# Kernel tuning notes

Measured on AMD Instinct MI355X. Metric: run time of the kernel, lower is better.

The kernel has to match this reference:

```python
import jax, jax.numpy as jnp
import numpy as np

EPS = 1.1920929e-07  # torch fp32 finfo eps (F.rms_norm default)

def apply_rotary_emb(x, cos, sin):
    # x: [..., L, hd]; cos/sin: [L, hd/2] broadcast over leading dims
    x1, x2 = jnp.split(x, 2, axis=-1)
    y1 = x1 * cos + x2 * sin
    y2 = -x1 * sin + x2 * cos
    return jnp.concatenate([y1, y2], axis=-1)

def rms_norm(x):
    ms = jnp.mean(x * x, axis=-1, keepdims=True)
    return x * jax.lax.rsqrt(ms + EPS)

def setup_inputs() -> dict:
    key = jax.random.key(0)
    ks = jax.random.split(key, 7)
    B, L, D, H = 4, 2048, 2048, 16
    hd = D // H
    x = jax.random.normal(ks[0], (B, L, D), dtype=jnp.float32)
    cos = jax.random.uniform(ks[1], (L, hd // 2), dtype=jnp.float32)
    sin = jax.random.uniform(ks[2], (L, hd // 2), dtype=jnp.float32)
    s = 1.0 / np.sqrt(D)
    Wq = jax.random.normal(ks[3], (D, D), dtype=jnp.float32) * s
    Wk = jax.random.normal(ks[4], (hd, D), dtype=jnp.float32) * s
    Wv = jax.random.normal(ks[5], (hd, D), dtype=jnp.float32) * s
    Wo = jax.random.normal(ks[6], (D, D), dtype=jnp.float32) * s
    return {"x": x, "cos": cos, "sin": sin, "Wq": Wq, "Wk": Wk, "Wv": Wv, "Wo": Wo}

def reference(x, cos, sin, Wq, Wk, Wv, Wo):
    B, L, D = x.shape
    hd = Wk.shape[0]
    H = D // hd
    q = (x @ Wq.T).reshape(B, L, H, hd).transpose(0, 2, 1, 3)   # [B,H,L,hd]
    k = x @ Wk.T                                                 # [B,L,hd] single KV head
    v = x @ Wv.T                                                 # [B,L,hd]
    q = rms_norm(apply_rotary_emb(q, cos, sin))
    k = rms_norm(apply_rotary_emb(k, cos, sin))
    new_k = k[:, None]  # [B,1,L,hd] cache layout
    new_v = v[:, None]
    scale = 1.0 / np.sqrt(hd).astype(np.float32)
    scores = jnp.einsum('bhqd,bkd->bhqk', q, k) * scale          # [B,H,L,L]
    causal = jnp.tril(jnp.ones((L, L), dtype=bool))
    scores = jnp.where(causal, scores, -jnp.inf)
    attn = jax.nn.softmax(scores, axis=-1)
    out = jnp.einsum('bhqk,bkd->bhqd', attn, v)                  # [B,H,L,hd]
    out = out.transpose(0, 2, 1, 3).reshape(B, L, D) @ Wo.T
    return (out, (new_k, new_v))
```

## Files before the change

kernel.cpp:

```cpp
#include <hip/hip_runtime.h>
#include <hip/hip_bf16.h>

typedef __hip_bfloat16 bf16;
typedef __attribute__((ext_vector_type(8))) short s8v;
typedef __attribute__((ext_vector_type(4))) short s4v;
typedef __attribute__((ext_vector_type(4))) float f4v;

#define B_  4
#define L_  2048
#define D_  2048
#define H_  16
#define HD_ 128

#define QSCALE 0.12751745f

__device__ __forceinline__ float ldm(const void* p, size_t i, int m) {
    return m ? ((const float*)p)[i]
             : __bfloat162float(((const bf16*)p)[i]);
}
__device__ __forceinline__ void stm(void* p, size_t i, int m, float v) {
    if (m) ((float*)p)[i] = v;
    else   ((bf16*)p)[i] = __float2bfloat16(v);
}

__device__ __forceinline__ void glds16(const bf16* g, bf16* l) {
    __builtin_amdgcn_global_load_lds(
        (const __attribute__((address_space(1))) void*)g,
        (__attribute__((address_space(3))) void*)l, 16, 0, 0);
}

__global__ __launch_bounds__(256) void cvt_kernel(
    const void* __restrict__ src, bf16* __restrict__ dst, int n8, int m)
{
    int i = blockIdx.x * 256 + threadIdx.x;
    if (i >= n8) return;
    if (m) {
        const f4v* p = (const f4v*)src + (size_t)i * 2;
        f4v a = p[0], b = p[1];
        bf16 t[8];
        #pragma unroll
        for (int e = 0; e < 4; e++) {
            t[e]     = __float2bfloat16(a[e]);
            t[4 + e] = __float2bfloat16(b[e]);
        }
        ((s8v*)dst)[i] = *(s8v*)&t[0];
    } else {
        ((s8v*)dst)[i] = ((const s8v*)src)[i];
    }
}

__global__ __launch_bounds__(256) void gemm_glds_kernel(
    const bf16* __restrict__ A, const bf16* __restrict__ Bw,
    void* __restrict__ C, size_t cOff, int cm, int N, int K)
{
    __shared__ bf16 a_lds[128 * 32];
    __shared__ bf16 b_lds[128 * 32];
    const int t = threadIdx.x;

    const int nbx = gridDim.x;
    const int id  = blockIdx.y * nbx + blockIdx.x;
    const int cpx = (nbx * (int)gridDim.y) >> 3;
    const int swz = (id & 7) * cpx + (id >> 3);
    const int n0  = (swz % nbx) * 128;
    const int m0  = (swz / nbx) * 128;

    const int w  = t >> 6, ln = t & 63;
    const int wr = w >> 1, wc = w & 1;
    const int fr = ln & 15, kg = ln >> 4;

    const int srow = w * 32 + (ln >> 2);
    const int scol = (ln & 3) * 8;
    const bf16* ga = A  + (size_t)(m0 + srow) * K + scol;
    const bf16* gb = Bw + (size_t)(n0 + srow) * K + scol;
    bf16* la = &a_lds[w * 1024];
    bf16* lb = &b_lds[w * 1024];

    f4v acc[4][4];
    #pragma unroll
    for (int i = 0; i < 4; i++)
        #pragma unroll
        for (int j = 0; j < 4; j++)
            #pragma unroll
            for (int r = 0; r < 4; r++) acc[i][j][r] = 0.f;

    for (int k0 = 0; k0 < K; k0 += 32) {
        __syncthreads();
        glds16(ga + k0,          la);
        glds16(ga + k0 + 16 * K, la + 512);
        glds16(gb + k0,          lb);
        glds16(gb + k0 + 16 * K, lb + 512);
        __syncthreads();

        s8v af[4], bfv[4];
        #pragma unroll
        for (int i = 0; i < 4; i++)
            af[i] = *(const s8v*)&a_lds[(wr * 64 + i * 16 + fr) * 32 + kg * 8];
        #pragma unroll
        for (int j = 0; j < 4; j++)
            bfv[j] = *(const s8v*)&b_lds[(wc * 64 + j * 16 + fr) * 32 + kg * 8];
        #pragma unroll
        for (int i = 0; i < 4; i++)
            #pragma unroll
            for (int j = 0; j < 4; j++)
                acc[i][j] = __builtin_amdgcn_mfma_f32_16x16x32_bf16(
                    af[i], bfv[j], acc[i][j], 0, 0, 0);
    }

    #pragma unroll
    for (int i = 0; i < 4; i++)
        #pragma unroll
        for (int j = 0; j < 4; j++)
            #pragma unroll
            for (int r = 0; r < 4; r++) {
                int row = m0 + wr * 64 + i * 16 + kg * 4 + r;
                int col = n0 + wc * 64 + j * 16 + fr;
                stm(C, cOff + (size_t)row * N + col, cm, acc[i][j][r]);
            }
}

__global__ __launch_bounds__(512, 2) void gemm256_kernel(
    const bf16* __restrict__ A, const bf16* __restrict__ Bw,
    void* __restrict__ C, size_t cOff, int cm, int N, int K)
{
    __shared__ __align__(16) bf16 a_lds[2][256 * 64];
    __shared__ __align__(16) bf16 b_lds[2][256 * 64];
    const int t = threadIdx.x;

    const int nbx = gridDim.x;
    const int id  = blockIdx.y * nbx + blockIdx.x;
    const int cpx = (nbx * (int)gridDim.y) >> 3;
    const int swz = (id & 7) * cpx + (id >> 3);
    const int n0  = (swz % nbx) * 256;
    const int m0  = (swz / nbx) * 256;

    const int w  = t >> 6, ln = t & 63;
    const int wr = w >> 2, wc = w & 3;
    const int fr = ln & 15, kg = ln >> 4;

    const int sb   = w * 256 + ln;
    const int srow = sb >> 3;
    const int scol = (sb & 7) * 8;
    const bf16* gA = A  + (size_t)(m0 + srow) * K + scol;
    const bf16* gB = Bw + (size_t)(n0 + srow) * K + scol;
    const int lbase = w * 2048;

    f4v acc[8][4];
    #pragma unroll
    for (int i = 0; i < 8; i++)
        #pragma unroll
        for (int j = 0; j < 4; j++)
            #pragma unroll
            for (int r = 0; r < 4; r++) acc[i][j][r] = 0.f;

    const int NT = K >> 6;

    #pragma unroll
    for (int u = 0; u < 4; u++) {
        glds16(gA + (size_t)(u * 8) * K, &a_lds[0][lbase + u * 512]);
        glds16(gB + (size_t)(u * 8) * K, &b_lds[0][lbase + u * 512]);
    }

    for (int kt = 0; kt < NT; ++kt) {
        const int cur = kt & 1;
        if (kt + 1 < NT) {
            const int nk = (kt + 1) << 6;
            #pragma unroll
            for (int u = 0; u < 4; u++) {
                glds16(gA + (size_t)(u * 8) * K + nk, &a_lds[cur ^ 1][lbase + u * 512]);
                glds16(gB + (size_t)(u * 8) * K + nk, &b_lds[cur ^ 1][lbase + u * 512]);
            }
            asm volatile("s_waitcnt vmcnt(8)" ::: "memory");
        } else {
            asm volatile("s_waitcnt vmcnt(0)" ::: "memory");
        }
        __builtin_amdgcn_s_barrier();

        #pragma unroll
        for (int kst = 0; kst < 2; kst++) {
            s8v af[8], bf[4];
            #pragma unroll
            for (int i = 0; i < 8; i++)
                af[i] = *(const s8v*)&a_lds[cur][(wr * 128 + i * 16 + fr) * 64
                                                + kst * 32 + kg * 8];
            #pragma unroll
            for (int j = 0; j < 4; j++)
                bf[j] = *(const s8v*)&b_lds[cur][(wc * 64 + j * 16 + fr) * 64
                                                + kst * 32 + kg * 8];
            #pragma unroll
            for (int i = 0; i < 8; i++)
                #pragma unroll
                for (int j = 0; j < 4; j++)
                    acc[i][j] = __builtin_amdgcn_mfma_f32_16x16x32_bf16(
                        af[i], bf[j], acc[i][j], 0, 0, 0);
        }
        asm volatile("s_waitcnt lgkmcnt(0)" ::: "memory");
        __builtin_amdgcn_s_barrier();
    }

    #pragma unroll
    for (int i = 0; i < 8; i++)
        #pragma unroll
        for (int j = 0; j < 4; j++)
            #pragma unroll
            for (int r = 0; r < 4; r++) {
                int row = m0 + wr * 128 + i * 16 + kg * 4 + r;
                int col = n0 + wc * 64 + j * 16 + fr;
                stm(C, cOff + (size_t)row * N + col, cm, acc[i][j][r]);
            }
}

__global__ __launch_bounds__(256) void rot_rms_kernel(
    bf16* __restrict__ p, int stride, int ldiv, float oscale,
    const void* __restrict__ cosb, const void* __restrict__ sinb, int em,
    bf16* __restrict__ kout, void* __restrict__ out2, int om)
{
    const int row  = blockIdx.x * 4 + (threadIdx.x >> 6);
    const int lane = threadIdx.x & 63;
    const int l    = (row / ldiv) % L_;
    bf16* pr = p + (size_t)row * stride;

    float x1 = __bfloat162float(pr[lane]);
    float x2 = __bfloat162float(pr[lane + 64]);
    float c  = ldm(cosb, (size_t)l * 64 + lane, em);
    float s  = ldm(sinb, (size_t)l * 64 + lane, em);
    float y1 =  x1 * c + x2 * s;
    float y2 = -x1 * s + x2 * c;

    float sq = y1 * y1 + y2 * y2;
    #pragma unroll
    for (int off = 32; off > 0; off >>= 1) sq += __shfl_xor(sq, off);
    float rinv = rsqrtf(sq * (1.0f / 128.0f) + 1.1920929e-07f);
    y1 *= rinv; y2 *= rinv;

    pr[lane]      = __float2bfloat16(y1 * oscale);
    pr[lane + 64] = __float2bfloat16(y2 * oscale);
    if (kout) {
        kout[(size_t)row * HD_ + lane]      = __float2bfloat16(y1);
        kout[(size_t)row * HD_ + lane + 64] = __float2bfloat16(y2);
    }
    if (out2) {
        stm(out2, (size_t)row * HD_ + lane,      om, y1);
        stm(out2, (size_t)row * HD_ + lane + 64, om, y2);
    }
}

__global__ __launch_bounds__(256) void transpose_v_kernel(
    const bf16* __restrict__ v, int vstride, int vcol0,
    bf16* __restrict__ vt, void* __restrict__ vout, int om)
{
    const int l0 = blockIdx.x * 32, c0 = blockIdx.y * 32, b = blockIdx.z;
    __shared__ bf16 tile[32][36];
    const int t = threadIdx.x;
    {
        int r = t >> 3, c4 = (t & 7) * 4;
        const bf16* src = v + (size_t)(b * L_ + l0 + r) * vstride + vcol0 + c0 + c4;
        s4v sv = *(const s4v*)src;
        *(s4v*)&tile[r][c4] = sv;
        size_t oidx = (size_t)(b * L_ + l0 + r) * HD_ + c0 + c4;
        if (om) {
            f4v f;
            #pragma unroll
            for (int e = 0; e < 4; e++) f[e] = __bfloat162float(((bf16*)&sv)[e]);
            *(f4v*)((float*)vout + oidx) = f;
        } else {
            *(s4v*)((bf16*)vout + oidx) = sv;
        }
    }
    __syncthreads();
    {
        int c = t >> 3, r4 = (t & 7) * 4;
        bf16 tmp[4];
        #pragma unroll
        for (int e = 0; e < 4; e++) tmp[e] = tile[r4 + e][c];
        *(s4v*)&vt[(size_t)(b * HD_ + c0 + c) * L_ + l0 + r4] = *(s4v*)&tmp[0];
    }
}

__global__ __launch_bounds__(256, 2) void attn_kernel(
    const bf16* __restrict__ q,
    const bf16* __restrict__ kbuf,
    const bf16* __restrict__ vt,
    bf16* __restrict__ o)
{
    const int bx = blockIdx.x;
    const int h  = blockIdx.y, b = blockIdx.z;
    const int t  = threadIdx.x, w = t >> 6, ln = t & 63;
    const int fr = ln & 15, kg = ln >> 4;

    __shared__ bf16 k_lds[64][132];
    __shared__ bf16 vt_lds[128][68];
    __shared__ bf16 p_lds[128][68];

    const int rK = t >> 2, cK = (t & 3) * 32;
    const int rV = t >> 1, cV = (t & 1) * 32;

    #pragma unroll 1
    for (int half = 0; half < 2; half++) {
        const int l0 = half ? (L_ - 128 - bx * 128) : bx * 128;

        s8v qf[2][4];
        #pragma unroll
        for (int s = 0; s < 2; s++) {
            size_t base = (size_t)(b * L_ + l0 + w * 32 + s * 16 + fr) * D_
                          + h * HD_ + kg * 8;
            #pragma unroll
            for (int kst = 0; kst < 4; kst++)
                qf[s][kst] = *(const s8v*)(q + base + kst * 32);
        }

        float m_i[2] = {-3.0e38f, -3.0e38f};
        float l_i[2] = {0.f, 0.f};
        f4v o_acc[8][2];
        #pragma unroll
        for (int mt = 0; mt < 8; mt++)
            #pragma unroll
            for (int s = 0; s < 2; s++)
                #pragma unroll
                for (int r = 0; r < 4; r++) o_acc[mt][s][r] = 0.f;

        const int qmax_w = l0 + w * 32 + 31;
        const int kend   = l0 + 128;

        for (int kb = 0; kb < kend; kb += 64) {
            s8v kr[4], vr[4];
            {
                const s8v* ks = (const s8v*)(kbuf + (size_t)(b * L_ + kb + rK) * HD_ + cK);
                const s8v* vs = (const s8v*)(vt + (size_t)(b * HD_ + rV) * L_ + kb + cV);
                #pragma unroll
                for (int u = 0; u < 4; u++) { kr[u] = ks[u]; vr[u] = vs[u]; }
            }
            __syncthreads();
            #pragma unroll
            for (int u = 0; u < 4; u++) {
                *(s8v*)&k_lds[rK][cK + u * 8]  = kr[u];
                *(s8v*)&vt_lds[rV][cV + u * 8] = vr[u];
            }
            __syncthreads();

            if (kb <= qmax_w) {
                f4v sacc[4][2];
                #pragma unroll
                for (int jm = 0; jm < 4; jm++)
                    #pragma unroll
                    for (int s = 0; s < 2; s++)
                        #pragma unroll
                        for (int r = 0; r < 4; r++) sacc[jm][s][r] = 0.f;

                __builtin_amdgcn_s_setprio(1);
                #pragma unroll
                for (int kst = 0; kst < 4; kst++) {
                    #pragma unroll
                    for (int jm = 0; jm < 4; jm++) {
                        s8v af = *(const s8v*)&k_lds[jm * 16 + fr][kst * 32 + kg * 8];
                        #pragma unroll
                        for (int s = 0; s < 2; s++)
                            sacc[jm][s] = __builtin_amdgcn_mfma_f32_16x16x32_bf16(
                                af, qf[s][kst], sacc[jm][s], 0, 0, 0);
                    }
                }
                __builtin_amdgcn_s_setprio(0);

                #pragma unroll
                for (int s = 0; s < 2; s++) {
                    const int qrow = l0 + w * 32 + s * 16 + fr;
                    float sv[4][4];
                    if (kb + 63 > l0 + w * 32 + s * 16) {
                        #pragma unroll
                        for (int jm = 0; jm < 4; jm++)
                            #pragma unroll
                            for (int r = 0; r < 4; r++) {
                                int key = kb + jm * 16 + kg * 4 + r;
                                sv[jm][r] = (key <= qrow) ? sacc[jm][s][r] : -3.0e38f;
                            }
                    } else {
                        #pragma unroll
                        for (int jm = 0; jm < 4; jm++)
                            #pragma unroll
                            for (int r = 0; r < 4; r++) sv[jm][r] = sacc[jm][s][r];
                    }
                    float mj[4];
                    #pragma unroll
                    for (int jm = 0; jm < 4; jm++)
                        mj[jm] = fmaxf(fmaxf(sv[jm][0], sv[jm][1]),
                                       fmaxf(sv[jm][2], sv[jm][3]));
                    float mx = fmaxf(fmaxf(mj[0], mj[1]), fmaxf(mj[2], mj[3]));
                    mx = fmaxf(mx, __shfl_xor(mx, 16));
                    mx = fmaxf(mx, __shfl_xor(mx, 32));

                    float mn = m_i[s];
                    if (!__all(mx - mn <= 8.0f)) {
                        float mnew  = fmaxf(mn, mx);
                        float alpha = exp2f(mn - mnew);
                        m_i[s] = mnew;
                        l_i[s] *= alpha;
                        #pragma unroll
                        for (int mt = 0; mt < 8; mt++)
                            #pragma unroll
                            for (int r = 0; r < 4; r++) o_acc[mt][s][r] *= alpha;
                        mn = mnew;
                    }

                    float rs0 = 0.f, rs1 = 0.f;
                    #pragma unroll
                    for (int jm = 0; jm < 4; jm++) {
                        float p0 = exp2f(sv[jm][0] - mn);
                        float p1 = exp2f(sv[jm][1] - mn);
                        float p2 = exp2f(sv[jm][2] - mn);
                        float p3 = exp2f(sv[jm][3] - mn);
                        rs0 += p0 + p2;
                        rs1 += p1 + p3;
                        bf16 pb[4];
                        pb[0] = __float2bfloat16(p0);
                        pb[1] = __float2bfloat16(p1);
                        pb[2] = __float2bfloat16(p2);
                        pb[3] = __float2bfloat16(p3);
                        *(s4v*)&p_lds[w * 32 + s * 16 + fr][jm * 16 + kg * 4] =
                            *(s4v*)&pb[0];
                    }
                    float rsum = rs0 + rs1;
                    rsum += __shfl_xor(rsum, 16);
                    rsum += __shfl_xor(rsum, 32);
                    l_i[s] += rsum;
                }

                __builtin_amdgcn_s_setprio(1);
                #pragma unroll
                for (int ks2 = 0; ks2 < 2; ks2++) {
                    s8v pf[2];
                    #pragma unroll
                    for (int s = 0; s < 2; s++)
                        pf[s] = *(const s8v*)&p_lds[w * 32 + s * 16 + fr][ks2 * 32 + kg * 8];
                    #pragma unroll
                    for (int mt = 0; mt < 8; mt++) {
                        s8v vf = *(const s8v*)&vt_lds[mt * 16 + fr][ks2 * 32 + kg * 8];
                        #pragma unroll
                        for (int s = 0; s < 2; s++)
                            o_acc[mt][s] = __builtin_amdgcn_mfma_f32_16x16x32_bf16(
                                vf, pf[s], o_acc[mt][s], 0, 0, 0);
                    }
                }
                __builtin_amdgcn_s_setprio(0);
            }
        }

        #pragma unroll
        for (int s = 0; s < 2; s++) {
            float rl = 1.f / l_i[s];
            size_t base = (size_t)(b * L_ + l0 + w * 32 + s * 16 + fr) * D_
                          + h * HD_ + kg * 4;
            #pragma unroll
            for (int mt = 0; mt < 8; mt++) {
                bf16 ob[4];
                #pragma unroll
                for (int r = 0; r < 4; r++)
                    ob[r] = __float2bfloat16(o_acc[mt][s][r] * rl);
                *(s4v*)(o + base + mt * 16) = *(s4v*)&ob[0];
            }
        }
    }
}

extern "C" void kernel_launch(void* const* d_in, const int* in_sizes, int n_in,
                              void* d_out, int out_size, void* d_ws, size_t ws_size,
                              hipStream_t stream)
{
    const void* x    = d_in[0];
    const void* cosb = d_in[1];
    const void* sinb = d_in[2];
    const void* Wq   = d_in[3];
    const void* Wk   = d_in[4];
    const void* Wv   = d_in[5];
    const void* Wo   = d_in[6];

    const size_t NX   = (size_t)B_ * L_ * D_;
    const size_t NW   = (size_t)D_ * D_;
    const size_t NWK  = (size_t)HD_ * D_;
    const size_t NKV  = (size_t)B_ * L_ * HD_;
    const size_t NOUT = NX + 2 * NKV;

    const int xm  = (in_sizes[0] == (int)(NX * 2))  ? 0 : 1;
    const int em  = (in_sizes[1] == (int)((size_t)L_ * 64 * 2)) ? 0 : 1;
    const int wm  = (in_sizes[3] == (int)(NW * 2))  ? 0 : 1;
    const int wkm = (in_sizes[4] == (int)(NWK * 2)) ? 0 : 1;
    const int om  = (out_size    == (int)(NOUT * 2)) ? 0 : 1;

    bf16* qbuf  = (bf16*)d_ws;
    bf16* kvbuf = qbuf  + NX;
    bf16* kbuf  = kvbuf + (size_t)B_ * L_ * 256;
    bf16* vtbuf = kbuf  + NKV;
    bf16* wkvb  = vtbuf + NKV;
    bf16* wwb   = kvbuf;

    const bf16* xb;
    if (xm) {
        cvt_kernel<<<(int)(NX / 8 / 256), 256, 0, stream>>>(x, (bf16*)d_out, (int)(NX / 8), 1);
        xb = (const bf16*)d_out;
    } else {
        xb = (const bf16*)x;
    }

    const bf16* wq;
    if (wm) {
        cvt_kernel<<<(int)(NW / 8 / 256), 256, 0, stream>>>(Wq, wwb, (int)(NW / 8), 1);
        wq = wwb;
    } else {
        wq = (const bf16*)Wq;
    }
    cvt_kernel<<<(int)(NWK / 8 / 256), 256, 0, stream>>>(Wk, wkvb,       (int)(NWK / 8), wkm);
    cvt_kernel<<<(int)(NWK / 8 / 256), 256, 0, stream>>>(Wv, wkvb + NWK, (int)(NWK / 8), wkm);

    gemm256_kernel<<<dim3(D_ / 256, (B_ * L_) / 256), 512, 0, stream>>>(
        xb, wq, qbuf, 0, 0, D_, D_);
    gemm_glds_kernel<<<dim3(256 / 128, (B_ * L_) / 128), 256, 0, stream>>>(
        xb, wkvb, kvbuf, 0, 0, 256, D_);

    rot_rms_kernel<<<(B_ * L_ * H_) / 4, 256, 0, stream>>>(
        qbuf, HD_, H_, QSCALE, cosb, sinb, em, nullptr, nullptr, 0);
    char* d_out_b = (char*)d_out;
    void* kout2 = d_out_b + NX * (om ? 4 : 2);
    rot_rms_kernel<<<(B_ * L_) / 4, 256, 0, stream>>>(
        kvbuf, 256, 1, 1.0f, cosb, sinb, em, kbuf, kout2, om);

    void* vout2 = d_out_b + (NX + NKV) * (om ? 4 : 2);
    transpose_v_kernel<<<dim3(L_ / 32, HD_ / 32, B_), 256, 0, stream>>>(
        kvbuf, 256, 128, vtbuf, vout2, om);

    attn_kernel<<<dim3(L_ / 256, H_, B_), 256, 0, stream>>>(
        qbuf, kbuf, vtbuf, qbuf);

    const bf16* wo;
    if (wm) {
        cvt_kernel<<<(int)(NW / 8 / 256), 256, 0, stream>>>(Wo, wwb, (int)(NW / 8), 1);
        wo = wwb;
    } else {
        wo = (const bf16*)Wo;
    }
    gemm256_kernel<<<dim3(D_ / 256, (B_ * L_) / 256), 512, 0, stream>>>(
        qbuf, wo, d_out, 0, om, D_, D_);
}
```

Before: 521.4 us.

## Split GEMM K-tile into half-tiles with finer-grained staged prefetch

Restructures the 256x256 GEMM main loop so each 64-wide K tile is stored as two 32-wide halves, and global-to-LDS loads are issued per half-tile, interleaved between MFMA groups. Waits use vmcnt on outstanding half-tile units, and s_setprio brackets the MFMA bursts. The aim is to overlap memory loads with compute more evenly and reduce stalls at barriers. It adds more barriers and waitcnt bookkeeping, and the vmcnt counts must match the number of outstanding loads exactly or the loop will read stale data.

Measured after the change: 502.8 us. 1.04x faster.

```diff
diff --git a/kernel.cpp b/kernel.cpp
--- a/kernel.cpp
+++ b/kernel.cpp
@@ -118,12 +118,25 @@
             }
 }
 
+__device__ __forceinline__ void stage_unit(
+    const bf16* __restrict__ G, int row0, int k0, int K,
+    bf16* lds, int w, int ln)
+{
+    #pragma unroll
+    for (int u = 0; u < 2; u++) {
+        int blk = u * 8 + w;
+        int r   = blk * 16 + (ln >> 2);
+        int ck  = (ln & 3) * 8;
+        glds16(G + (size_t)(row0 + r) * K + k0 + ck, lds + blk * 512);
+    }
+}
+
 __global__ __launch_bounds__(512, 2) void gemm256_kernel(
     const bf16* __restrict__ A, const bf16* __restrict__ Bw,
     void* __restrict__ C, size_t cOff, int cm, int N, int K)
 {
-    __shared__ __align__(16) bf16 a_lds[2][256 * 64];
-    __shared__ __align__(16) bf16 b_lds[2][256 * 64];
+    __shared__ __align__(16) bf16 a_lds[2][2][256 * 32];
+    __shared__ __align__(16) bf16 b_lds[2][2][256 * 32];
     const int t = threadIdx.x;
 
     const int nbx = gridDim.x;
@@ -137,13 +150,6 @@
     const int wr = w >> 2, wc = w & 3;
     const int fr = ln & 15, kg = ln >> 4;
 
-    const int sb   = w * 256 + ln;
-    const int srow = sb >> 3;
-    const int scol = (sb & 7) * 8;
-    const bf16* gA = A  + (size_t)(m0 + srow) * K + scol;
-    const bf16* gB = Bw + (size_t)(n0 + srow) * K + scol;
-    const int lbase = w * 2048;
-
     f4v acc[8][4];
     #pragma unroll
     for (int i = 0; i < 8; i++)
@@ -154,47 +160,96 @@
 
     const int NT = K >> 6;
 
-    #pragma unroll
-    for (int u = 0; u < 4; u++) {
-        glds16(gA + (size_t)(u * 8) * K, &a_lds[0][lbase + u * 512]);
-        glds16(gB + (size_t)(u * 8) * K, &b_lds[0][lbase + u * 512]);
+    stage_unit(A,  m0, 0,  K, &a_lds[0][0][0], w, ln);
+    stage_unit(Bw, n0, 0,  K, &b_lds[0][0][0], w, ln);
+    stage_unit(A,  m0, 32, K, &a_lds[0][1][0], w, ln);
+    stage_unit(Bw, n0, 32, K, &b_lds[0][1][0], w, ln);
+    if (NT > 1) {
+        stage_unit(A,  m0, 64, K, &a_lds[1][0][0], w, ln);
+        stage_unit(Bw, n0, 64, K, &b_lds[1][0][0], w, ln);
     }
 
     for (int kt = 0; kt < NT; ++kt) {
-        const int cur = kt & 1;
-        if (kt + 1 < NT) {
-            const int nk = (kt + 1) << 6;
-            #pragma unroll
-            for (int u = 0; u < 4; u++) {
-                glds16(gA + (size_t)(u * 8) * K + nk, &a_lds[cur ^ 1][lbase + u * 512]);
-                glds16(gB + (size_t)(u * 8) * K + nk, &b_lds[cur ^ 1][lbase + u * 512]);
-            }
-            asm volatile("s_waitcnt vmcnt(8)" ::: "memory");
-        } else {
-            asm volatile("s_waitcnt vmcnt(0)" ::: "memory");
-        }
+        const int c = kt & 1, nb = c ^ 1;
+        if (kt + 1 < NT) asm volatile("s_waitcnt vmcnt(8)" ::: "memory");
+        else             asm volatile("s_waitcnt vmcnt(4)" ::: "memory");
         __builtin_amdgcn_s_barrier();
 
-        #pragma unroll
-        for (int kst = 0; kst < 2; kst++) {
-            s8v af[8], bf[4];
+        if (kt + 1 < NT)
+            stage_unit(A, m0, (kt + 1) * 64 + 32, K, &a_lds[nb][1][0], w, ln);
+        {
+            s8v af[8], bfv[4];
             #pragma unroll
             for (int i = 0; i < 8; i++)
-                af[i] = *(const s8v*)&a_lds[cur][(wr * 128 + i * 16 + fr) * 64
-                                                + kst * 32 + kg * 8];
-            #pragma unroll
-            for (int j = 0; j < 4; j++)
-                bf[j] = *(const s8v*)&b_lds[cur][(wc * 64 + j * 16 + fr) * 64
-                                                + kst * 32 + kg * 8];
+                af[i] = *(const s8v*)&a_lds[c][0][(wr * 128 + i * 16 + fr) * 32 + kg * 8];
+            #pragma unroll
+            for (int j = 0; j < 2; j++)
+                bfv[j] = *(const s8v*)&b_lds[c][0][(wc * 64 + j * 16 + fr) * 32 + kg * 8];
+            asm volatile("s_waitcnt lgkmcnt(0)" ::: "memory");
+            __builtin_amdgcn_s_setprio(1);
             #pragma unroll
             for (int i = 0; i < 8; i++)
                 #pragma unroll
-                for (int j = 0; j < 4; j++)
+                for (int j = 0; j < 2; j++)
                     acc[i][j] = __builtin_amdgcn_mfma_f32_16x16x32_bf16(
-                        af[i], bf[j], acc[i][j], 0, 0, 0);
-        }
-        asm volatile("s_waitcnt lgkmcnt(0)" ::: "memory");
+                        af[i], bfv[j], acc[i][j], 0, 0, 0);
+            __builtin_amdgcn_s_setprio(0);
+
+            if (kt + 1 < NT)
+                stage_unit(Bw, n0, (kt + 1) * 64 + 32, K, &b_lds[nb][1][0], w, ln);
+            #pragma unroll
+            for (int j = 2; j < 4; j++)
+                bfv[j] = *(const s8v*)&b_lds[c][0][(wc * 64 + j * 16 + fr) * 32 + kg * 8];
+            asm volatile("s_waitcnt lgkmcnt(0)" ::: "memory");
+            __builtin_amdgcn_s_setprio(1);
+            #pragma unroll
+            for (int i = 0; i < 8; i++)
+                #pragma unroll
+                for (int j = 2; j < 4; j++)
+                    acc[i][j] = __builtin_amdgcn_mfma_f32_16x16x32_bf16(
+                        af[i], bfv[j], acc[i][j], 0, 0, 0);
+            __builtin_amdgcn_s_setprio(0);
+        }
+
+        if (kt + 1 < NT) asm volatile("s_waitcnt vmcnt(8)" ::: "memory");
+        else             asm volatile("s_waitcnt vmcnt(0)" ::: "memory");
         __builtin_amdgcn_s_barrier();
+
+        if (kt + 2 < NT)
+            stage_unit(A, m0, (kt + 2) * 64, K, &a_lds[c][0][0], w, ln);
+        {
+            s8v af[8], bfv[4];
+            #pragma unroll
+            for (int i = 0; i < 8; i++)
+                af[i] = *(const s8v*)&a_lds[c][1][(wr * 128 + i * 16 + fr) * 32 + kg * 8];
+            #pragma unroll
+            for (int j = 0; j < 2; j++)
+                bfv[j] = *(const s8v*)&b_lds[c][1][(wc * 64 + j * 16 + fr) * 32 + kg * 8];
+            asm volatile("s_waitcnt lgkmcnt(0)" ::: "memory");
+            __builtin_amdgcn_s_setprio(1);
+            #pragma unroll
+            for (int i = 0; i < 8; i++)
+                #pragma unroll
+                for (int j = 0; j < 2; j++)
+                    acc[i][j] = __builtin_amdgcn_mfma_f32_16x16x32_bf16(
+                        af[i], bfv[j], acc[i][j], 0, 0, 0);
+            __builtin_amdgcn_s_setprio(0);
+
+            if (kt + 2 < NT)
+                stage_unit(Bw, n0, (kt + 2) * 64, K, &b_lds[c][0][0], w, ln);
+            #pragma unroll
+            for (int j = 2; j < 4; j++)
+                bfv[j] = *(const s8v*)&b_lds[c][1][(wc * 64 + j * 16 + fr) * 32 + kg * 8];
+            asm volatile("s_waitcnt lgkmcnt(0)" ::: "memory");
+            __builtin_amdgcn_s_setprio(1);
+            #pragma unroll
+            for (int i = 0; i < 8; i++)
+                #pragma unroll
+                for (int j = 2; j < 4; j++)
+                    acc[i][j] = __builtin_amdgcn_mfma_f32_16x16x32_bf16(
+                        af[i], bfv[j], acc[i][j], 0, 0, 0);
+            __builtin_amdgcn_s_setprio(0);
+        }
     }
 
     #pragma unroll
```
